# Kernel tuning notes

Measured on AMD Instinct MI355X. Metric: run time of the kernel, lower is better.

## Reference

```python
import jax, jax.numpy as jnp
import numpy as np

EMB = 12
NUM_CLASSES = 17
NUM_GRAPHS = 1000


def gcn_conv(h, W, b, row, col, n):
    # h: [N, Fin]; row/col already include self-loops. Aggregation at col (target).
    h = h @ W + b  # [N, Fout]
    deg = jax.ops.segment_sum(jnp.ones_like(col, dtype=h.dtype), col, num_segments=n)
    dinv = deg ** -0.5  # self-loops guarantee deg >= 1
    norm = dinv[row] * dinv[col]  # [E]
    msg = norm[:, None] * h[row]  # gather + scale
    return jax.ops.segment_sum(msg, col, num_segments=n)  # scatter-add


def setup_inputs() -> dict:
    key = jax.random.key(0)
    ks = jax.random.split(key, 16)
    N, E = 400000, 6400000
    x = jax.random.normal(ks[0], (N, 4), dtype=jnp.float32)
    edge_index = jax.random.randint(ks[1], (2, E), 0, N, dtype=jnp.int64)
    batch_index = jnp.sort(jax.random.randint(ks[2], (N,), 0, NUM_GRAPHS, dtype=jnp.int64))

    def lin(k, fi, fo):
        k1, k2 = jax.random.split(k)
        bound = 1.0 / np.sqrt(fi)
        W = jax.random.uniform(k1, (fi, fo), minval=-bound, maxval=bound, dtype=jnp.float32)
        b = jax.random.uniform(k2, (fo,), minval=-bound, maxval=bound, dtype=jnp.float32)
        return W, b

    W0, b0 = lin(ks[3], 4, EMB)
    W1, b1 = lin(ks[4], EMB, EMB)
    W2, b2 = lin(ks[5], EMB, EMB)
    W3, b3 = lin(ks[6], EMB, EMB)
    Wout, bout = lin(ks[7], EMB * 2, NUM_CLASSES)
    return {"x": x, "edge_index": edge_index, "batch_index": batch_index,
            "W0": W0, "b0": b0, "W1": W1, "b1": b1, "W2": W2, "b2": b2,
            "W3": W3, "b3": b3, "Wout": Wout, "bout": bout}


def reference(x, edge_index, batch_index, W0, b0, W1, b1, W2, b2, W3, b3, Wout, bout):
    n = x.shape[0]
    loops = jnp.arange(n, dtype=edge_index.dtype)
    row = jnp.concatenate([edge_index[0], loops])
    col = jnp.concatenate([edge_index[1], loops])

    h = jnp.tanh(gcn_conv(x, W0, b0, row, col, n))
    h = jnp.tanh(gcn_conv(h, W1, b1, row, col, n))
    h = jnp.tanh(gcn_conv(h, W2, b2, row, col, n))
    h = jnp.tanh(gcn_conv(h, W3, b3, row, col, n))

    gmax = jax.ops.segment_max(h, batch_index, num_segments=NUM_GRAPHS)
    gsum = jax.ops.segment_sum(h, batch_index, num_segments=NUM_GRAPHS)
    cnt = jax.ops.segment_sum(jnp.ones((n,), dtype=h.dtype), batch_index, num_segments=NUM_GRAPHS)
    gmean = gsum / jnp.maximum(cnt, 1.0)[:, None]
    hidden = jnp.concatenate([gmax, gmean], axis=1)  # [G, 2*EMB]
    out = hidden @ Wout + bout  # [G, NUM_CLASSES]
    return out, hidden
```

## Files before the change

kernel.cpp:

```cpp
#include <hip/hip_runtime.h>
#include <hip/hip_bf16.h>
#include <math.h>

typedef __hip_bfloat16 bf16;

#define EMB 12
#define NCLS 17
#define NG 1000
#define BSHIFT 9
#define BSPAN 512
#define MAXNB 1024
#define CHUNK 16384
#define EB 8
#define TSHIFT 16
#define NTILE 8
#define NKEY (BSPAN*NTILE)

__device__ __forceinline__ float b2f(bf16 v){ return __bfloat162float(v); }

__device__ __forceinline__ unsigned short f2bf_rne(float f){
  unsigned int u = __float_as_uint(f);
  unsigned int r = (u + 0x7FFFu + ((u >> 16) & 1u)) >> 16;
  return (unsigned short)r;
}

__device__ __forceinline__ float ldf(const void* p, size_t i, int isbf){
  if (isbf) return b2f(((const bf16*)p)[i]);
  return ((const float*)p)[i];
}
__device__ __forceinline__ void stout(void* p, size_t i, float v, int isbf){
  if (isbf) ((unsigned short*)p)[i] = f2bf_rne(v);
  else      ((float*)p)[i] = v;
}

__device__ __forceinline__ void rowload(const float* p, float o[12]){
  const float4* q = (const float4*)p;
  float4 a = q[0], b = q[1], c = q[2];
  o[0]=a.x;o[1]=a.y;o[2]=a.z;o[3]=a.w;o[4]=b.x;o[5]=b.y;o[6]=b.z;o[7]=b.w;
  o[8]=c.x;o[9]=c.y;o[10]=c.z;o[11]=c.w;
}
__device__ __forceinline__ void rowload(const bf16* p, float o[12]){
  const uint4* q = (const uint4*)p;
  uint4 u0 = q[0];
  uint2 u1 = *(const uint2*)(q+1);
  o[0] =__uint_as_float(u0.x<<16); o[1] =__uint_as_float(u0.x&0xFFFF0000u);
  o[2] =__uint_as_float(u0.y<<16); o[3] =__uint_as_float(u0.y&0xFFFF0000u);
  o[4] =__uint_as_float(u0.z<<16); o[5] =__uint_as_float(u0.z&0xFFFF0000u);
  o[6] =__uint_as_float(u0.w<<16); o[7] =__uint_as_float(u0.w&0xFFFF0000u);
  o[8] =__uint_as_float(u1.x<<16); o[9] =__uint_as_float(u1.x&0xFFFF0000u);
  o[10]=__uint_as_float(u1.y<<16); o[11]=__uint_as_float(u1.y&0xFFFF0000u);
}
__device__ __forceinline__ void rowstore(float* p, const float o[12]){
  float4* q = (float4*)p;
  q[0] = make_float4(o[0],o[1],o[2],o[3]);
  q[1] = make_float4(o[4],o[5],o[6],o[7]);
  q[2] = make_float4(o[8],o[9],o[10],o[11]);
}
__device__ __forceinline__ void rowstore(bf16* p, const float o[12]){
  unsigned int u[6];
  #pragma unroll
  for (int k=0;k<6;k++)
    u[k] = (unsigned int)f2bf_rne(o[2*k]) | ((unsigned int)f2bf_rne(o[2*k+1])<<16);
  uint2* q = (uint2*)p;
  q[0] = make_uint2(u[0],u[1]);
  q[1] = make_uint2(u[2],u[3]);
  q[2] = make_uint2(u[4],u[5]);
}

__global__ void k_detect(const int* __restrict__ ei, const unsigned short* __restrict__ xh,
                         int* __restrict__ flags){
  if (blockIdx.x==0 && threadIdx.x==0){
    int z = 1;
    for (int k=1; k<32; k+=2) z &= (ei[k]==0);
    flags[0] = z;
    int hits = 0;
    for (int k=0; k<32; k+=2){
      int e = (xh[k] >> 7) & 0xFF;
      if (e >= 100 && e <= 140) hits++;
    }
    flags[1] = (hits >= 12) ? 1 : 0;
  }
}
__device__ __forceinline__ int ld_row(const int* ei, long long E, long long i, int w64){
  return w64 ? ei[2*i] : ei[i];
}
__device__ __forceinline__ int ld_col(const int* ei, long long E, long long i, int w64){
  return w64 ? ei[2*E + 2*i] : ei[E + i];
}
__device__ __forceinline__ int ld_batch(const int* b, long long i, int w64){
  return w64 ? b[2*i] : b[i];
}

__global__ void k_zero_i(int* __restrict__ p, int n){
  int i = blockIdx.x*blockDim.x + threadIdx.x;
  if (i < n) p[i] = 0;
}
__global__ void __launch_bounds__(256)
k_bkt_count(const int* __restrict__ ei, const int* __restrict__ flags,
            int* __restrict__ bcnt, int* __restrict__ bofs, int E, int NB){
  __shared__ int h[MAXNB];
  int t = threadIdx.x;
  for (int j=t; j<NB; j+=256) h[j] = 0;
  __syncthreads();
  int w64 = flags[0];
  long long base = (long long)blockIdx.x * CHUNK;
  for (int k0=0; k0<CHUNK; k0+=256*EB){
    int c[EB]; bool v[EB];
    #pragma unroll
    for (int u=0;u<EB;u++){
      long long i = base + k0 + u*256 + t;
      v[u] = (i < E);
      c[u] = v[u] ? ld_col(ei, E, i, w64) : 0;
    }
    #pragma unroll
    for (int u=0;u<EB;u++) if (v[u]) atomicAdd(&h[c[u]>>BSHIFT], 1);
  }
  __syncthreads();
  size_t rowb = (size_t)blockIdx.x * NB;
  for (int j=t; j<NB; j+=256){
    int c = h[j];
    bofs[rowb + j] = c;
    if (c > 0) atomicAdd(&bcnt[j], c);
  }
}
__global__ void __launch_bounds__(1024)
k_bkt_scan_par(const int* __restrict__ bcnt, int* __restrict__ bbase,
               int* __restrict__ rs2, int NB, int NBK){
  __shared__ int s[1024];
  int t = threadIdx.x;
  int v = (t < NB) ? bcnt[t] : 0;
  s[t] = v;
  __syncthreads();
  for (int off=1; off<1024; off<<=1){
    int add = (t >= off) ? s[t-off] : 0;
    __syncthreads();
    s[t] += add;
    __syncthreads();
  }
  if (t < NB) bbase[t] = s[t] - v;
  if (t == 1023){
    bbase[NB] = s[1023];
    rs2[NBK]  = s[1023];
  }
}
__global__ void __launch_bounds__(256)
k_colscan(int* __restrict__ bofs, const int* __restrict__ bbase, int NB, int GC){
  __shared__ int part[256];
  int j = blockIdx.x, t = threadIdx.x;
  int K = (GC + 255) / 256;
  int beg = t*K, end = beg+K < GC ? beg+K : GC;
  int s = 0;
  for (int i=beg; i<end; i++) s += bofs[(size_t)i*NB + j];
  part[t] = s;
  __syncthreads();
  for (int off=1; off<256; off<<=1){
    int add = (t >= off) ? part[t-off] : 0;
    __syncthreads();
    part[t] += add;
    __syncthreads();
  }
  int run = bbase[j] + part[t] - s;
  for (int i=beg; i<end; i++){
    size_t idx = (size_t)i*NB + j;
    int v = bofs[idx];
    bofs[idx] = run;
    run += v;
  }
}
__global__ void __launch_bounds__(256)
k_bkt_place(const int* __restrict__ ei, const int* __restrict__ flags,
            const int* __restrict__ bofs, int* __restrict__ pairs, int E, int NB){
  __shared__ int h[MAXNB];
  int t = threadIdx.x;
  size_t rowb = (size_t)blockIdx.x * NB;
  for (int j=t; j<NB; j+=256) h[j] = bofs[rowb + j];
  __syncthreads();
  int w64 = flags[0];
  long long base = (long long)blockIdx.x * CHUNK;
  for (int k0=0; k0<CHUNK; k0+=256*EB){
    int r[EB], c[EB]; bool v[EB];
    #pragma unroll
    for (int u=0;u<EB;u++){
      long long i = base + k0 + u*256 + t;
      v[u] = (i < E);
      r[u] = v[u] ? ld_row(ei, E, i, w64) : 0;
      c[u] = v[u] ? ld_col(ei, E, i, w64) : 0;
    }
    int pos[EB];
    #pragma unroll
    for (int u=0;u<EB;u++) pos[u] = v[u] ? atomicAdd(&h[c[u]>>BSHIFT], 1) : 0;
    #pragma unroll
    for (int u=0;u<EB;u++)
      if (v[u]) pairs[pos[u]] = r[u] | ((r[u]>>TSHIFT)<<19) | ((c[u] & (BSPAN-1)) << 22);
  }
}
__device__ __forceinline__ int tkey(int pk){
  return (((pk>>19)&7)<<BSHIFT) | (pk>>22);
}
__global__ void __launch_bounds__(256)
k_group(const int* __restrict__ pairs, const int* __restrict__ bbase,
        float* __restrict__ dinv, int* __restrict__ src,
        int* __restrict__ rs2, int N){
  __shared__ int cnt[NKEY];
  __shared__ int cur[NKEY];
  __shared__ int part[256];
  int b = blockIdx.x, t = threadIdx.x;
  int lo = bbase[b], hi = bbase[b+1];
  #pragma unroll
  for (int u=0;u<NKEY/256;u++) cnt[u*256+t] = 0;
  __syncthreads();
  {
    int p = lo + t;
    for (; p + 3*256 < hi; p += 4*256){
      int k0=tkey(pairs[p]), k1=tkey(pairs[p+256]), k2=tkey(pairs[p+512]), k3=tkey(pairs[p+768]);
      atomicAdd(&cnt[k0],1); atomicAdd(&cnt[k1],1);
      atomicAdd(&cnt[k2],1); atomicAdd(&cnt[k3],1);
    }
    for (; p < hi; p += 256) atomicAdd(&cnt[tkey(pairs[p])],1);
  }
  __syncthreads();
  int loc[16]; int s = 0;
  #pragma unroll
  for (int u=0;u<16;u++){ loc[u] = cnt[t*16+u]; s += loc[u]; }
  part[t] = s;
  __syncthreads();
  for (int off=1; off<256; off<<=1){
    int add = (t >= off) ? part[t-off] : 0;
    __syncthreads();
    part[t] += add;
    __syncthreads();
  }
  int run = lo + part[t] - s;
  #pragma unroll
  for (int u=0;u<16;u++){ cur[t*16+u] = run; run += loc[u]; }
  __syncthreads();
  {
    size_t rb = (size_t)b * NKEY;
    #pragma unroll
    for (int u=0;u<16;u++){ int k = t*16+u; rs2[rb + k] = cur[k]; }
    int col0 = b << BSHIFT;
    #pragma unroll
    for (int u=0;u<2;u++){
      int j = 2*t + u;
      int colg = col0 + j;
      if (colg < N){
        int deg = 0;
        #pragma unroll
        for (int tt=0; tt<NTILE; tt++) deg += cnt[(tt<<BSHIFT) | j];
        dinv[colg] = rsqrtf((float)deg + 1.0f);
      }
    }
  }
  __syncthreads();
  {
    int p = lo + t;
    for (; p + 3*256 < hi; p += 4*256){
      int pk0=pairs[p], pk1=pairs[p+256], pk2=pairs[p+512], pk3=pairs[p+768];
      int q0 = atomicAdd(&cur[tkey(pk0)], 1);
      int q1 = atomicAdd(&cur[tkey(pk1)], 1);
      int q2 = atomicAdd(&cur[tkey(pk2)], 1);
      int q3 = atomicAdd(&cur[tkey(pk3)], 1);
      src[q0] = pk0 & 0x7FFFF; src[q1] = pk1 & 0x7FFFF;
      src[q2] = pk2 & 0x7FFFF; src[q3] = pk3 & 0x7FFFF;
    }
    for (; p < hi; p += 256){
      int pk = pairs[p];
      int q = atomicAdd(&cur[tkey(pk)], 1);
      src[q] = pk & 0x7FFFF;
    }
  }
}

template<typename GT>
__global__ void k_lin_first(const void* __restrict__ x, const void* __restrict__ W,
                            const void* __restrict__ b, const int* __restrict__ flags,
                            const float* __restrict__ dinv,
                            GT* __restrict__ g, int n){
  __shared__ float Ws[4*EMB];
  __shared__ float bs[EMB];
  int t = threadIdx.x;
  int isbf = flags[1];
  if (t < 4*EMB) Ws[t] = ldf(W, t, isbf);
  if (t < EMB)   bs[t] = ldf(b, t, isbf);
  __syncthreads();
  int i = blockIdx.x*blockDim.x + t;
  if (i >= n) return;
  float xi[4];
  #pragma unroll
  for (int k=0;k<4;k++) xi[k] = ldf(x, (size_t)i*4+k, isbf);
  float d = dinv[i];
  float o[12];
  #pragma unroll
  for (int j=0;j<EMB;j++){
    float h = bs[j];
    #pragma unroll
    for (int k=0;k<4;k++) h = fmaf(xi[k], Ws[k*EMB+j], h);
    o[j] = d*h;
  }
  rowstore(g + (size_t)i*16, o);
}

template<typename GT>
__global__ void k_lin_mid(const float* __restrict__ acc, const void* __restrict__ W,
                          const void* __restrict__ b, const int* __restrict__ flags,
                          const float* __restrict__ dinv,
                          GT* __restrict__ g, int n){
  __shared__ float Ws[EMB*EMB];
  __shared__ float bs[EMB];
  int t = threadIdx.x;
  int isbf = flags[1];
  if (t < EMB*EMB) Ws[t] = ldf(W, t, isbf);
  if (t < EMB)     bs[t] = ldf(b, t, isbf);
  __syncthreads();
  int i = blockIdx.x*blockDim.x + t;
  if (i >= n) return;
  float xi[EMB];
  size_t abase = (size_t)i*EMB;
  #pragma unroll
  for (int k=0;k<EMB;k++) xi[k] = tanhf(acc[abase+k]);
  float d = dinv[i];
  float o[12];
  #pragma unroll
  for (int j=0;j<EMB;j++){
    float h = bs[j];
    #pragma unroll
    for (int k=0;k<EMB;k++) h = fmaf(xi[k], Ws[k*EMB+j], h);
    o[j] = d*h;
  }
  rowstore(g + (size_t)i*16, o);
}

template<typename GT>
__device__ __forceinline__ void seg_tail(const GT* __restrict__ gin,
                                         const int* __restrict__ src,
                                         int p, int e, float a[12]){
  for (; p+1 < e; p += 2){
    int r0 = src[p], r1 = src[p+1];
    float h0[12], h1[12];
    rowload(gin + (size_t)r0*16, h0);
    rowload(gin + (size_t)r1*16, h1);
    #pragma unroll
    for (int j=0;j<12;j++) a[j] += h0[j] + h1[j];
  }
  if (p < e){
    int r = src[p];
    float h[12];
    rowload(gin + (size_t)r*16, h);
    #pragma unroll
    for (int j=0;j<12;j++) a[j] += h[j];
  }
}

template<typename GT>
__device__ __forceinline__ void seg_sum2(const GT* __restrict__ gin,
                                         const int* __restrict__ src,
                                         int p0, int e0, int p1, int e1,
                                         float a0[12], float a1[12]){
  while (p0+1 < e0 && p1+1 < e1){
    int r00 = src[p0], r01 = src[p0+1], r10 = src[p1], r11 = src[p1+1];
    float h00[12], h01[12], h10[12], h11[12];
    rowload(gin + (size_t)r00*16, h00);
    rowload(gin + (size_t)r01*16, h01);
    rowload(gin + (size_t)r10*16, h10);
    rowload(gin + (size_t)r11*16, h11);
    #pragma unroll
    for (int j=0;j<12;j++){ a0[j] += h00[j]+h01[j]; a1[j] += h10[j]+h11[j]; }
    p0 += 2; p1 += 2;
  }
  seg_tail<GT>(gin, src, p0, e0, a0);
  seg_tail<GT>(gin, src, p1, e1, a1);
}

template<typename GT, int MODE>
__device__ __forceinline__ void finish_col(int c, int n, const float a[12],
                                           const GT* __restrict__ gin,
                                           const float* __restrict__ dinv,
                                           const float* Ws, const float* bs,
                                           void* __restrict__ outp){
  if (c >= n) return;
  float v[12];
  rowload(gin + (size_t)c*16, v);
  #pragma unroll
  for (int j=0;j<12;j++) v[j] += a[j];
  float d = dinv[c];
  if (MODE == 0){
    float h[12];
    #pragma unroll
    for (int k=0;k<12;k++) h[k] = tanhf(d*v[k]);
    float o[12];
    #pragma unroll
    for (int j=0;j<12;j++){
      float w = bs[j];
      #pragma unroll
      for (int k=0;k<12;k++) w = fmaf(h[k], Ws[k*EMB+j], w);
      o[j] = d*w;
    }
    rowstore((GT*)outp + (size_t)c*16, o);
  } else {
    float4* ap = (float4*)((float*)outp + (size_t)c*EMB);
    ap[0] = make_float4(tanhf(d*v[0]), tanhf(d*v[1]), tanhf(d*v[2]),  tanhf(d*v[3]));
    ap[1] = make_float4(tanhf(d*v[4]), tanhf(d*v[5]), tanhf(d*v[6]),  tanhf(d*v[7]));
    ap[2] = make_float4(tanhf(d*v[8]), tanhf(d*v[9]), tanhf(d*v[10]), tanhf(d*v[11]));
  }
}

template<typename GT, int MODE>
__global__ void __launch_bounds__(256)
k_gather_rot(const int* __restrict__ rs2, const int* __restrict__ src,
             const float* __restrict__ dinv, const GT* __restrict__ gin,
             const void* __restrict__ W, const void* __restrict__ b,
             const int* __restrict__ flags, void* __restrict__ outp,
             int n, int nt){
  __shared__ float Ws[EMB*EMB];
  __shared__ float bs[EMB];
  int t = threadIdx.x;
  if (MODE == 0){
    int isbf = flags[1];
    if (t < EMB*EMB) Ws[t] = ldf(W, t, isbf);
    if (t < EMB)     bs[t] = ldf(b, t, isbf);
    __syncthreads();
  }
  int c0 = blockIdx.x*512 + t;
  int c1 = c0 + 256;
  bool v0 = (c0 < n), v1 = (c1 < n);
  int q0 = v0 ? c0 : 0, q1 = v1 ? c1 : 0;
  int base0 = ((q0>>BSHIFT)<<12) + (q0 & (BSPAN-1));
  int base1 = ((q1>>BSHIFT)<<12) + (q1 & (BSPAN-1));
  float a0[12], a1[12];
  #pragma unroll
  for (int j=0;j<12;j++){ a0[j]=0.f; a1[j]=0.f; }
  int tau = (int)(blockIdx.x & 7) % nt;
  int i0 = base0 + (tau<<BSHIFT);
  int i1 = base1 + (tau<<BSHIFT);
  int s0 = rs2[i0], e0 = rs2[i0+1];
  int s1 = rs2[i1], e1 = rs2[i1+1];
  for (int k=0; k<nt; k++){
    int tn = tau+1; if (tn >= nt) tn = 0;
    int ps0=0, pe0=0, ps1=0, pe1=0;
    if (k+1 < nt){
      int ni0 = base0 + (tn<<BSHIFT);
      int ni1 = base1 + (tn<<BSHIFT);
      ps0 = rs2[ni0]; pe0 = rs2[ni0+1];
      ps1 = rs2[ni1]; pe1 = rs2[ni1+1];
    }
    seg_sum2<GT>(gin, src, s0, e0, s1, e1, a0, a1);
    s0=ps0; e0=pe0; s1=ps1; e1=pe1; tau=tn;
  }
  finish_col<GT,MODE>(c0, n, a0, gin, dinv, Ws, bs, outp);
  finish_col<GT,MODE>(c1, n, a1, gin, dinv, Ws, bs, outp);
}

__global__ void k_cnt_deg(const int* __restrict__ ei, const int* __restrict__ flags,
                          int* __restrict__ cnt, int e){
  int i = blockIdx.x*blockDim.x + threadIdx.x;
  if (i >= e) return;
  atomicAdd(&cnt[ld_col(ei, e, i, flags[0])], 1);
}
__global__ void k_dinv_from_cnt(const int* __restrict__ cnt, float* __restrict__ dinv, int n){
  int i = blockIdx.x*blockDim.x + threadIdx.x;
  if (i < n) dinv[i] = rsqrtf((float)(cnt[i] + 1));
}
__global__ void k_selfinit(const float* __restrict__ g, const float* __restrict__ dinv,
                           float* __restrict__ acc, int n){
  int i = blockIdx.x*blockDim.x + threadIdx.x;
  if (i >= n) return;
  float d = dinv[i];
  float h[12]; rowload(g + (size_t)i*16, h);
  #pragma unroll
  for (int j=0;j<EMB;j++) acc[(size_t)i*EMB+j] = d*h[j];
}
__global__ void k_scatter(const int* __restrict__ ei, const int* __restrict__ flags,
                          const float* __restrict__ dinv, const float* __restrict__ g,
                          float* __restrict__ acc, int e){
  int i = blockIdx.x*blockDim.x + threadIdx.x;
  if (i >= e) return;
  int w64 = flags[0];
  int r = ld_row(ei, e, i, w64);
  int c = ld_col(ei, e, i, w64);
  float w = dinv[c];
  float h[12];
  rowload(g + (size_t)r*16, h);
  float* ap = acc + (size_t)c*EMB;
  #pragma unroll
  for (int j=0;j<EMB;j++) atomicAdd(ap+j, w*h[j]);
}

template<int DOTANH>
__global__ void __launch_bounds__(256)
k_pool(const float* __restrict__ acc, const int* __restrict__ batch,
       const int* __restrict__ flags,
       const void* __restrict__ Wout, const void* __restrict__ bout,
       void* __restrict__ out, int n){
  int g = blockIdx.x;
  int w64  = flags[0];
  int isbf = flags[1];
  __shared__ int se[2];
  __shared__ float smax[4][EMB];
  __shared__ float ssum[4][EMB];
  __shared__ float hid[2*EMB];
  if (threadIdx.x == 0){
    int lo=0, hi=n;
    while (lo<hi){ int m=(lo+hi)>>1; if (ld_batch(batch,m,w64) < g) lo=m+1; else hi=m; }
    se[0]=lo;
    int lo2=lo; hi=n;
    while (lo2<hi){ int m=(lo2+hi)>>1; if (ld_batch(batch,m,w64) < g+1) lo2=m+1; else hi=m; }
    se[1]=lo2;
  }
  __syncthreads();
  int start=se[0], end=se[1];
  float lmax[EMB], lsum[EMB];
  #pragma unroll
  for (int j=0;j<EMB;j++){ lmax[j]=-3.0e38f; lsum[j]=0.f; }
  for (int i=start+(int)threadIdx.x; i<end; i+=blockDim.x){
    size_t base=(size_t)i*EMB;
    #pragma unroll
    for (int j=0;j<EMB;j++){
      float h = DOTANH ? tanhf(acc[base+j]) : acc[base+j];
      lmax[j] = fmaxf(lmax[j], h);
      lsum[j] += h;
    }
  }
  #pragma unroll
  for (int m=32;m>=1;m>>=1){
    #pragma unroll
    for (int j=0;j<EMB;j++){
      lmax[j] = fmaxf(lmax[j], __shfl_xor(lmax[j], m, 64));
      lsum[j] += __shfl_xor(lsum[j], m, 64);
    }
  }
  int wave = threadIdx.x>>6, lane = threadIdx.x&63;
  if (lane==0){
    #pragma unroll
    for (int j=0;j<EMB;j++){ smax[wave][j]=lmax[j]; ssum[wave][j]=lsum[j]; }
  }
  __syncthreads();
  int cnt = end-start;
  if (threadIdx.x < EMB){
    int j = threadIdx.x;
    float mx=smax[0][j], sm=ssum[0][j];
    #pragma unroll
    for (int w=1;w<4;w++){ mx=fmaxf(mx,smax[w][j]); sm+=ssum[w][j]; }
    if (cnt <= 0){ mx = 0.f; sm = 0.f; }
    float mean = sm / fmaxf((float)cnt, 1.0f);
    hid[j]     = mx;
    hid[EMB+j] = mean;
    stout(out, (size_t)NG*NCLS + (size_t)g*2*EMB + j,       mx,   isbf);
    stout(out, (size_t)NG*NCLS + (size_t)g*2*EMB + EMB + j, mean, isbf);
  }
  __syncthreads();
  if (threadIdx.x < NCLS){
    int c = threadIdx.x;
    float o = ldf(bout, c, isbf);
    #pragma unroll
    for (int k=0;k<2*EMB;k++) o = fmaf(hid[k], ldf(Wout, (size_t)k*NCLS+c, isbf), o);
    stout(out, (size_t)g*NCLS + c, o, isbf);
  }
}

__global__ void k_zero_out_noflags(void* __restrict__ out, int m){
  int i = blockIdx.x*blockDim.x + threadIdx.x;
  if (i < m) ((float*)out)[i] = 0.0f;
}

static void build_csr(const int* ei, const void* x, int* flags, int* bcnt, int* bbase,
                      int* bofs, float* dinv, int* src, int* pairs, int* rs2,
                      int N, int E, int NB, hipStream_t stream){
  const int TB = 256;
  const int gc = (E + CHUNK - 1) / CHUNK;
  const int NBK = NB * NKEY;
  k_detect      <<<1, 64, 0, stream>>>(ei, (const unsigned short*)x, flags);
  k_zero_i      <<<(NB+TB-1)/TB, TB, 0, stream>>>(bcnt, NB);
  k_bkt_count   <<<gc, TB, 0, stream>>>(ei, flags, bcnt, bofs, E, NB);
  k_bkt_scan_par<<<1, 1024, 0, stream>>>(bcnt, bbase, rs2, NB, NBK);
  k_colscan     <<<NB, TB, 0, stream>>>(bofs, bbase, NB, gc);
  k_bkt_place   <<<gc, TB, 0, stream>>>(ei, flags, bofs, pairs, E, NB);
  k_group       <<<NB, TB, 0, stream>>>(pairs, bbase, dinv, src, rs2, N);
}

static size_t alignup(size_t v){ return (v + 63) & ~(size_t)63; }
static size_t maxsz(size_t a, size_t b){ return a > b ? a : b; }

extern "C" void kernel_launch(void* const* d_in, const int* in_sizes, int n_in,
                              void* d_out, int out_size, void* d_ws, size_t ws_size,
                              hipStream_t stream) {
  const void* x     = d_in[0];
  const int*  ei    = (const int*)d_in[1];
  const int*  batch = (const int*)d_in[2];
  const void* W0 = d_in[3];  const void* b0 = d_in[4];
  const void* W1 = d_in[5];  const void* b1 = d_in[6];
  const void* W2 = d_in[7];  const void* b2 = d_in[8];
  const void* W3 = d_in[9];  const void* b3 = d_in[10];
  const void* Wout = d_in[11]; const void* bout = d_in[12];

  const int N = in_sizes[0] / 4;
  const int E = in_sizes[1] / 2;
  const int NB = (N + BSPAN - 1) >> BSHIFT;
  const int GC = (E + CHUNK - 1) / CHUNK;
  const int TB = 256;
  const int gn = (N + TB - 1) / TB;
  const int gr = (N + 511) / 512;
  const int nt = (N + (1<<TSHIFT) - 1) >> TSHIFT;

  char* base = (char*)d_ws;

  size_t o_flags  = 0;
  size_t o_dinv   = alignup(o_flags + 64);
  size_t o_bcnt   = alignup(o_dinv + (size_t)N*4);
  size_t o_bbase  = alignup(o_bcnt + (size_t)NB*4);
  size_t o_bofs   = alignup(o_bbase + ((size_t)NB+1)*4);
  size_t o_rs2    = alignup(o_bofs + (size_t)GC*NB*4);
  size_t o_src    = alignup(o_rs2 + ((size_t)NB*NKEY + 1)*4);
  size_t o_buf    = alignup(o_src + (size_t)E*4);

  int* flags  = (int*)(base+o_flags);
  float* dinv = (float*)(base+o_dinv);
  int* bcnt   = (int*)(base+o_bcnt);
  int* bbase  = (int*)(base+o_bbase);
  int* bofs   = (int*)(base+o_bofs);
  int* rs2    = (int*)(base+o_rs2);
  int* src    = (int*)(base+o_src);
  int* pairs  = (int*)(base+o_buf);

  bool fast_ok = (N < (1<<19)) && (NB <= MAXNB) && (nt <= NTILE);

  {
    size_t szR0 = maxsz((size_t)N*16*2, (size_t)N*EMB*4);
    size_t o_gB = alignup(o_buf + szR0);
    size_t need = o_gB + (size_t)N*16*2;
    bool pairs_fit = (size_t)E*4 <= need - o_buf;
    if (fast_ok && pairs_fit && ws_size >= need){
      bf16*  gA  = (bf16*)(base+o_buf);
      bf16*  gB  = (bf16*)(base+o_gB);
      float* acc = (float*)(base+o_buf);
      build_csr(ei, x, flags, bcnt, bbase, bofs, dinv, src, pairs, rs2, N, E, NB, stream);
      k_lin_first<bf16><<<gn, TB, 0, stream>>>(x, W0, b0, flags, dinv, gA, N);
      k_gather_rot<bf16,0><<<gr, TB, 0, stream>>>(rs2, src, dinv, gA, W1, b1, flags, gB, N, nt);
      k_gather_rot<bf16,0><<<gr, TB, 0, stream>>>(rs2, src, dinv, gB, W2, b2, flags, gA, N, nt);
      k_gather_rot<bf16,0><<<gr, TB, 0, stream>>>(rs2, src, dinv, gA, W3, b3, flags, gB, N, nt);
      k_gather_rot<bf16,1><<<gr, TB, 0, stream>>>(rs2, src, dinv, gB, 0, 0, flags, acc, N, nt);
      k_pool<0><<<NG, 256, 0, stream>>>(acc, batch, flags, Wout, bout, d_out, N);
      return;
    }
  }

  {
    size_t o_gA = o_buf;
    size_t o_gB = alignup(o_gA + (size_t)N*16*4);
    size_t need = o_gB + (size_t)N*16*4;
    bool pairs_fit = (size_t)E*4 <= need - o_buf;
    if (fast_ok && pairs_fit && ws_size >= need){
      float* gA  = (float*)(base+o_gA);
      float* gB  = (float*)(base+o_gB);
      float* acc = gA;
      build_csr(ei, x, flags, bcnt, bbase, bofs, dinv, src, pairs, rs2, N, E, NB, stream);
      k_lin_first<float><<<gn, TB, 0, stream>>>(x, W0, b0, flags, dinv, gA, N);
      k_gather_rot<float,0><<<gr, TB, 0, stream>>>(rs2, src, dinv, gA, W1, b1, flags, gB, N, nt);
      k_gather_rot<float,0><<<gr, TB, 0, stream>>>(rs2, src, dinv, gB, W2, b2, flags, gA, N, nt);
      k_gather_rot<float,0><<<gr, TB, 0, stream>>>(rs2, src, dinv, gA, W3, b3, flags, gB, N, nt);
      k_gather_rot<float,1><<<gr, TB, 0, stream>>>(rs2, src, dinv, gB, 0, 0, flags, acc, N, nt);
      k_pool<0><<<NG, 256, 0, stream>>>(acc, batch, flags, Wout, bout, d_out, N);
      return;
    }
  }

  {
    size_t f_cnt  = alignup(o_dinv + (size_t)N*4);
    size_t f_g    = alignup(f_cnt + (size_t)N*4);
    size_t f_acc  = alignup(f_g + (size_t)N*16*4);
    size_t f_end  = f_acc + (size_t)N*EMB*4;
    const int ge = (E + TB - 1) / TB;
    int* cnt = (int*)(base+f_cnt);

    if (ws_size >= f_end){
      float* g   = (float*)(base+f_g);
      float* acc = (float*)(base+f_acc);
      k_detect  <<<1, 64, 0, stream>>>(ei, (const unsigned short*)x, flags);
      k_zero_i  <<<gn, TB, 0, stream>>>(cnt, N);
      k_cnt_deg <<<ge, TB, 0, stream>>>(ei, flags, cnt, E);
      k_dinv_from_cnt<<<gn, TB, 0, stream>>>(cnt, dinv, N);
      k_lin_first<float><<<gn, TB, 0, stream>>>(x, W0, b0, flags, dinv, g, N);
      k_selfinit <<<gn, TB, 0, stream>>>(g, dinv, acc, N);
      k_scatter  <<<ge, TB, 0, stream>>>(ei, flags, dinv, g, acc, E);
      const void* Wl[3] = {W1,W2,W3};
      const void* bl[3] = {b1,b2,b3};
      for (int l=0;l<3;l++){
        k_lin_mid<float><<<gn, TB, 0, stream>>>(acc, Wl[l], bl[l], flags, dinv, g, N);
        k_selfinit<<<gn, TB, 0, stream>>>(g, dinv, acc, N);
        k_scatter <<<ge, TB, 0, stream>>>(ei, flags, dinv, g, acc, E);
      }
      k_pool<1><<<NG, 256, 0, stream>>>(acc, batch, flags, Wout, bout, d_out, N);
    } else {
      k_zero_out_noflags<<<(out_size+255)/256, 256, 0, stream>>>(d_out, out_size);
    }
  }
}
```

Baseline: 600.9 us.

## Stage bucket scatter through shared memory for coalesced global writes

The bucket placement kernel now counts each chunk's edges per bucket locally, prefix-sums those counts, and stages the packed pairs in shared memory sorted by bucket. It then writes them to global memory in order, so each bucket's pairs go out as a contiguous run. The chunk size is halved so the staging arrays fit in LDS. The grouping kernel likewise stages its per-tile source indices in shared memory when the bucket fits in a fixed capacity, then writes them out contiguously. The aim is to replace scattered global stores with coalesced ones, at the cost of an extra read pass over the column indices, larger LDS footprint and lower occupancy.

```diff
diff --git a/kernel.cpp b/kernel.cpp
--- a/kernel.cpp
+++ b/kernel.cpp
@@ -10,11 +10,12 @@
 #define BSHIFT 9
 #define BSPAN 512
 #define MAXNB 1024
-#define CHUNK 16384
+#define CHUNK 8192
 #define EB 8
 #define TSHIFT 16
 #define NTILE 8
 #define NKEY (BSPAN*NTILE)
+#define SCAP 11264
 
 __device__ __forceinline__ float b2f(bf16 v){ return __bfloat162float(v); }
 
@@ -170,13 +171,50 @@
 __global__ void __launch_bounds__(256)
 k_bkt_place(const int* __restrict__ ei, const int* __restrict__ flags,
             const int* __restrict__ bofs, int* __restrict__ pairs, int E, int NB){
-  __shared__ int h[MAXNB];
+  __shared__ int hb[MAXNB];
+  __shared__ int lcur[MAXNB];
+  __shared__ int part[256];
+  __shared__ int vals[CHUNK];
+  __shared__ int dst[CHUNK];
   int t = threadIdx.x;
   size_t rowb = (size_t)blockIdx.x * NB;
-  for (int j=t; j<NB; j+=256) h[j] = bofs[rowb + j];
+  for (int j=t; j<NB; j+=256){ hb[j] = bofs[rowb + j]; lcur[j] = 0; }
   __syncthreads();
   int w64 = flags[0];
   long long base = (long long)blockIdx.x * CHUNK;
+  long long rem = E - base;
+  int total = (rem < CHUNK) ? (int)rem : CHUNK;
+  for (int k0=0; k0<CHUNK; k0+=256*EB){
+    int c[EB]; bool v[EB];
+    #pragma unroll
+    for (int u=0;u<EB;u++){
+      long long i = base + k0 + u*256 + t;
+      v[u] = (i < E);
+      c[u] = v[u] ? ld_col(ei, E, i, w64) : 0;
+    }
+    #pragma unroll
+    for (int u=0;u<EB;u++) if (v[u]) atomicAdd(&lcur[c[u]>>BSHIFT], 1);
+  }
+  __syncthreads();
+  int loc[4]; int s = 0;
+  #pragma unroll
+  for (int u=0;u<4;u++){ int j=t*4+u; loc[u] = (j<NB) ? lcur[j] : 0; s += loc[u]; }
+  part[t] = s;
+  __syncthreads();
+  for (int off=1; off<256; off<<=1){
+    int add = (t >= off) ? part[t-off] : 0;
+    __syncthreads();
+    part[t] += add;
+    __syncthreads();
+  }
+  int run = part[t] - s;
+  #pragma unroll
+  for (int u=0;u<4;u++){
+    int j=t*4+u;
+    if (j<NB){ lcur[j] = run; hb[j] -= run; }
+    run += loc[u];
+  }
+  __syncthreads();
   for (int k0=0; k0<CHUNK; k0+=256*EB){
     int r[EB], c[EB]; bool v[EB];
     #pragma unroll
@@ -186,13 +224,18 @@
       r[u] = v[u] ? ld_row(ei, E, i, w64) : 0;
       c[u] = v[u] ? ld_col(ei, E, i, w64) : 0;
     }
-    int pos[EB];
-    #pragma unroll
-    for (int u=0;u<EB;u++) pos[u] = v[u] ? atomicAdd(&h[c[u]>>BSHIFT], 1) : 0;
-    #pragma unroll
-    for (int u=0;u<EB;u++)
-      if (v[u]) pairs[pos[u]] = r[u] | ((r[u]>>TSHIFT)<<19) | ((c[u] & (BSPAN-1)) << 22);
-  }
+    #pragma unroll
+    for (int u=0;u<EB;u++){
+      if (v[u]){
+        int j = c[u]>>BSHIFT;
+        int p = atomicAdd(&lcur[j], 1);
+        vals[p] = r[u] | ((r[u]>>TSHIFT)<<19) | ((c[u] & (BSPAN-1)) << 22);
+        dst[p]  = hb[j] + p;
+      }
+    }
+  }
+  __syncthreads();
+  for (int s2=t; s2<total; s2+=256) pairs[dst[s2]] = vals[s2];
 }
 __device__ __forceinline__ int tkey(int pk){
   return (((pk>>19)&7)<<BSHIFT) | (pk>>22);
@@ -204,8 +247,10 @@
   __shared__ int cnt[NKEY];
   __shared__ int cur[NKEY];
   __shared__ int part[256];
+  __shared__ int stage[SCAP];
   int b = blockIdx.x, t = threadIdx.x;
   int lo = bbase[b], hi = bbase[b+1];
+  int cap = hi - lo;
   #pragma unroll
   for (int u=0;u<NKEY/256;u++) cnt[u*256+t] = 0;
   __syncthreads();
@@ -252,7 +297,25 @@
     }
   }
   __syncthreads();
-  {
+  if (cap <= SCAP){
+    int p = lo + t;
+    for (; p + 3*256 < hi; p += 4*256){
+      int pk0=pairs[p], pk1=pairs[p+256], pk2=pairs[p+512], pk3=pairs[p+768];
+      int q0 = atomicAdd(&cur[tkey(pk0)], 1);
+      int q1 = atomicAdd(&cur[tkey(pk1)], 1);
+      int q2 = atomicAdd(&cur[tkey(pk2)], 1);
+      int q3 = atomicAdd(&cur[tkey(pk3)], 1);
+      stage[q0-lo] = pk0 & 0x7FFFF; stage[q1-lo] = pk1 & 0x7FFFF;
+      stage[q2-lo] = pk2 & 0x7FFFF; stage[q3-lo] = pk3 & 0x7FFFF;
+    }
+    for (; p < hi; p += 256){
+      int pk = pairs[p];
+      int q = atomicAdd(&cur[tkey(pk)], 1);
+      stage[q-lo] = pk & 0x7FFFF;
+    }
+    __syncthreads();
+    for (int s2=t; s2<cap; s2+=256) src[lo+s2] = stage[s2];
+  } else {
     int p = lo + t;
     for (; p + 3*256 < hi; p += 4*256){
       int pk0=pairs[p], pk1=pairs[p+256], pk2=pairs[p+512], pk3=pairs[p+768];
```

After: 553.5 us. 1.09x faster.
